# Kernel optimization log

Measured on AMD Instinct MI355X. Metric: run time of the kernel, lower is better.

The kernel has to match this reference:

```python
import jax, jax.numpy as jnp
import numpy as np

RCUT, RCUT_SMTH = 6.0, 0.5
SEL = [32, 64]
SEC = [0, 32, 96]
PAIRS = [(0, 0), (0, 1), (1, 1)]  # (ti, tj) with ti <= tj, matching stacked weight index
NF, NLOC, NALL = 1, 256, 512
NNEI = sum(SEL)
NG = 96


def setup_inputs() -> dict:
    key = jax.random.key(0)
    ks = jax.random.split(key, 10)
    # coords in a 4A cube so most neighbor distances are inside rcut=6
    extended_coord = jax.random.uniform(ks[0], (NF, NALL * 3), dtype=jnp.float32) * 4.0
    nl = jax.random.randint(ks[1], (NF, NLOC, NNEI), 0, NALL - 1)
    # shift indices >= own local index by 1 to avoid self-neighbors (zero distance)
    nlist = nl + (nl >= jnp.arange(NLOC)[None, :, None]).astype(nl.dtype)
    extended_atype = jax.random.randint(ks[2], (NF, NALL), 0, 2)
    mean = jnp.zeros((2, NNEI, 4), jnp.float32)
    stddev = jnp.ones((2, NNEI, 4), jnp.float32)
    def w(k, shape, fan):
        return jax.random.normal(k, shape, jnp.float32) / np.float32(np.sqrt(fan))
    W1 = w(ks[3], (3, 1, 24), 1.0)
    b1 = 0.1 * jax.random.normal(ks[4], (3, 24), jnp.float32)
    W2 = w(ks[5], (3, 24, 48), 24.0)
    b2 = 0.1 * jax.random.normal(ks[6], (3, 48), jnp.float32)
    W3 = w(ks[7], (3, 48, 96), 48.0)
    b3 = 0.1 * jax.random.normal(ks[8], (3, 96), jnp.float32)
    return dict(nlist=nlist, extended_coord=extended_coord, extended_atype=extended_atype,
                mean=mean, stddev=stddev, W1=W1, b1=b1, W2=W2, b2=b2, W3=W3, b3=b3)


def _smooth_weight(r, rmin, rmax):
    uu = (r - rmin) / (rmax - rmin)
    vv = uu * uu * uu * (-6.0 * uu * uu + 15.0 * uu - 10.0) + 1.0
    return jnp.where(r <= rmin, 1.0, jnp.where(r >= rmax, 0.0, vv))


def _env_mat(nlist, coord, atype, mean, stddev):
    nf, nloc, nnei = nlist.shape
    coord = coord.reshape(nf, -1, 3)
    mask = nlist >= 0
    nl = jnp.where(mask, nlist, 0)
    # gather neighbor coords: nf x nloc x nnei x 3
    coord_r = jnp.take_along_axis(coord, nl.reshape(nf, -1, 1), axis=1).reshape(nf, nloc, nnei, 3)
    diff = coord_r - coord[:, :nloc, None, :]
    length = jnp.linalg.norm(diff, axis=-1, keepdims=True)
    length = length + (~mask)[..., None].astype(diff.dtype)  # avoid 0-div on padded entries
    t0 = 1.0 / length
    t1 = diff / (length * length)
    sw = _smooth_weight(length, RCUT_SMTH, RCUT) * mask[..., None].astype(diff.dtype)
    env = jnp.concatenate([t0, t1], axis=-1) * sw  # nf x nloc x nnei x 4
    loc_type = atype[:, :nloc]
    dmatrix = (env - mean[loc_type]) / stddev[loc_type]
    return dmatrix, sw


def _embed(x, W1, b1, W2, b2, W3, b3):
    # EmbeddingNet 1->24->48->96, tanh, resnet doubling residuals
    h1 = jnp.tanh(x @ W1 + b1)
    h2 = jnp.tanh(h1 @ W2 + b2) + jnp.concatenate([h1, h1], axis=-1)
    h3 = jnp.tanh(h2 @ W3 + b3) + jnp.concatenate([h2, h2], axis=-1)
    return h3


def reference(nlist, extended_coord, extended_atype, mean, stddev, W1, b1, W2, b2, W3, b3):
    nf, nloc, nnei = nlist.shape
    dmatrix, sw = _env_mat(nlist, extended_coord, extended_atype, mean, stddev)
    dm = dmatrix.reshape(nf * nloc, nnei, 4)
    result = jnp.zeros((nf * nloc, NG), dm.dtype)
    for p, (ti, tj) in enumerate(PAIRS):
        rr_i = dm[:, SEC[ti]:SEC[ti + 1], 1:]  # nfnl x nt_i x 3
        rr_j = dm[:, SEC[tj]:SEC[tj + 1], 1:]  # nfnl x nt_j x 3
        env_ij = jnp.einsum('ijm,ikm->ijk', rr_i, rr_j)  # nfnl x nt_i x nt_j
        gg = _embed(env_ij[..., None], W1[p], b1[p], W2[p], b2[p], W3[p], b3[p])
        res_ij = jnp.einsum('ijk,ijkm->im', env_ij, gg)
        result = result + res_ij * (1.0 / (SEL[ti] * SEL[tj]))
    return result.reshape(nf, nloc, NG)
```

## Files before the change

### kernel.cpp

```cpp
#include <hip/hip_runtime.h>

#define NLOC 256
#define NNEI 96
#define NG   96
#define H1W  28
#define H2W  52
#define S2LE 2.88539008177793f

typedef __attribute__((ext_vector_type(8))) short short8;
typedef __attribute__((ext_vector_type(4))) float f32x4;
union Frag { uint4 u; short8 s; };

__device__ __forceinline__ float tanh_sc(float s) {
    float e = __builtin_amdgcn_exp2f(s);
    return 1.0f - 2.0f * __builtin_amdgcn_rcpf(e + 1.0f);
}
__device__ __forceinline__ unsigned short f2bf(float f) {
    unsigned int u = __float_as_uint(f);
    u += 0x7FFFu + ((u >> 16) & 1u);
    return (unsigned short)(u >> 16);
}
__device__ __forceinline__ unsigned short f2bf_rhu(float f) {
    return (unsigned short)((__float_as_uint(f) + 0x8000u) >> 16);
}
__device__ __forceinline__ unsigned int pack_bf2(float lo, float hi) {
    unsigned int a = __float_as_uint(lo) + 0x8000u;
    unsigned int b = __float_as_uint(hi) + 0x8000u;
    return __builtin_amdgcn_perm(b, a, 0x07060302);
}

__global__ __launch_bounds__(256) void prep_kernel(
        const float* __restrict__ W1, const float* __restrict__ b1,
        const float* __restrict__ W2, const float* __restrict__ b2,
        const float* __restrict__ W3, const float* __restrict__ b3,
        unsigned short* __restrict__ wf2, unsigned short* __restrict__ wf3,
        unsigned short* __restrict__ wfJ,
        float* __restrict__ w1s, float* __restrict__ b1s,
        float* __restrict__ b2s, float* __restrict__ b3s) {
    int t = blockIdx.x * blockDim.x + threadIdx.x;
    if (t < 2880) {
        int p = t / 960;
        int r = t % 960;
        int tile = r / 64;
        int l = r % 64;
        int nlo = l & 15, g = l >> 4;
        short8 v;
        if (tile < 3) {
            int nt = tile;
            #pragma unroll
            for (int j = 0; j < 8; j++) {
                int k = g * 8 + j;
                float w = (k < 24) ? W2[(p * 24 + k) * 48 + nt * 16 + nlo] * S2LE : 0.0f;
                v[j] = (short)f2bf(w);
            }
            *(short8*)(wf2 + ((p * 3 + nt) * 64 + l) * 8) = v;
        } else {
            int tt = tile - 3;
            int nt = tt >> 1, kc = tt & 1;
            #pragma unroll
            for (int j = 0; j < 8; j++) {
                int kk = (kc == 0) ? (g * 8 + j) : ((j < 4) ? (32 + g * 4 + j) : -1);
                float w = (kk >= 0) ? W3[(p * 48 + kk) * 96 + nt * 16 + nlo] * S2LE : 0.0f;
                v[j] = (short)f2bf(w);
            }
            *(short8*)(wf3 + ((p * 12 + nt * 2 + kc) * 64 + l) * 8) = v;
        }
    } else if (t < 3264) {
        int t2 = t - 2880;
        int f = t2 >> 6, l = t2 & 63;
        int ml = l & 15, g = l >> 4;
        short8 v;
        if (f < 3) {
            int c24 = (f * 16 + ml) % 24;
            #pragma unroll
            for (int j = 0; j < 8; j++)
                v[j] = (short)((g * 8 + j == c24) ? 0x3F80 : 0);
        } else {
            int nt2 = f - 3;
            if (nt2 < 2) {
                int c = nt2 * 16 + ml;
                #pragma unroll
                for (int j = 0; j < 8; j++)
                    v[j] = (short)((g * 8 + j == c) ? 0x3F80 : 0);
            } else {
                #pragma unroll
                for (int j = 0; j < 8; j++)
                    v[j] = (short)((j < 4 && (g * 4 + j) == ml) ? 0x3F80 : 0);
            }
        }
        *(short8*)(wfJ + (f * 64 + l) * 8) = v;
    } else if (t < 3768) {
        int u = t - 3264;
        if (u < 72)       { w1s[u] = W1[u] * S2LE; b1s[u] = b1[u] * S2LE; }
        else if (u < 216) { b2s[u - 72]  = b2[u - 72]  * S2LE; }
        else              { b3s[u - 216] = b3[u - 216] * S2LE; }
    }
}

__launch_bounds__(256, 4)
__global__ void mlp_kernel(const int* __restrict__ nlist, const float* __restrict__ coord,
                           const int* __restrict__ atype,
                           const float* __restrict__ mean, const float* __restrict__ stddev,
                           const float* __restrict__ w1s, const float* __restrict__ b1s,
                           const float* __restrict__ b2s, const float* __restrict__ b3s,
                           const unsigned short* __restrict__ wf2,
                           const unsigned short* __restrict__ wf3,
                           const unsigned short* __restrict__ wfJ,
                           float* __restrict__ out) {
    __shared__ __align__(16) unsigned char smem[40960];
    unsigned short* h1s = (unsigned short*)smem;
    unsigned short* h2s = (unsigned short*)(smem + 14336);
    float* rrl = (float*)(smem + 39808);
    unsigned char* h2b = (unsigned char*)h2s;

    int tid = threadIdx.x;
    int blk = blockIdx.x;
    int i = blk / 20;
    int b = blk - i * 20;

    int p, base_e, offi, offj, count, Aint;
    float scale;
    bool tri;
    if (b < 3)       { p=0; base_e=b*256;      offi=0;  offj=0;  scale=1.0f/1024.0f; count=528;  tri=true;  Aint=65;  }
    else if (b < 11) { p=1; base_e=(b-3)*256;  offi=0;  offj=32; scale=1.0f/2048.0f; count=2048; tri=false; Aint=0;   }
    else             { p=2; base_e=(b-11)*256; offi=32; offj=32; scale=1.0f/4096.0f; count=2080; tri=true;  Aint=129; }

    if (tid < NNEI) {
        int n = tid;
        int idx = nlist[i * NNEI + n];
        bool msk = idx >= 0;
        int safe = msk ? idx : 0;
        float cx = coord[i*3], cy = coord[i*3+1], cz = coord[i*3+2];
        float dx = coord[safe*3]   - cx;
        float dy = coord[safe*3+1] - cy;
        float dz = coord[safe*3+2] - cz;
        float rn = sqrtf(dx*dx + dy*dy + dz*dz) + (msk ? 0.0f : 1.0f);
        float sw;
        if (rn <= 0.5f)      sw = 1.0f;
        else if (rn >= 6.0f) sw = 0.0f;
        else {
            float uu = (rn - 0.5f) * (1.0f / 5.5f);
            sw = uu*uu*uu*(uu*(-6.0f*uu + 15.0f) - 10.0f) + 1.0f;
        }
        if (!msk) sw = 0.0f;
        float ir2 = 1.0f / (rn * rn);
        int ty = atype[i];
        const float* mu = mean   + (ty * NNEI + n) * 4;
        const float* sd = stddev + (ty * NNEI + n) * 4;
        rrl[n*3+0] = (dx * ir2 * sw - mu[1]) / sd[1];
        rrl[n*3+1] = (dy * ir2 * sw - mu[2]) / sd[2];
        rrl[n*3+2] = (dz * ir2 * sw - mu[3]) / sd[3];
    }
    __syncthreads();

    float xs;
    {
        int e = base_e + tid;
        bool valid = e < count;
        int ec = valid ? e : 0;
        int jj, kk;
        float mult = 1.0f;
        if (!tri) { jj = ec >> 6; kk = ec & 63; }
        else {
            float Af = (float)Aint;
            int j = (int)((Af - sqrtf(Af*Af - 8.0f*(float)ec)) * 0.5f);
            int Tj1 = ((j+1)*(Aint-j-1)) >> 1;
            if (ec >= Tj1) j++;
            int Tj = (j*(Aint-j)) >> 1;
            if (ec < Tj) { j--; Tj = (j*(Aint-j)) >> 1; }
            jj = j; kk = j + (ec - Tj);
            mult = (jj == kk) ? 1.0f : 2.0f;
        }
        const float* ri = rrl + (offi + jj) * 3;
        const float* rj = rrl + (offj + kk) * 3;
        float x = ri[0]*rj[0] + ri[1]*rj[1] + ri[2]*rj[2];
        x = valid ? x : 0.0f;
        xs = x * mult;

        const float* w1 = w1s + p * 24;
        const float* c1 = b1s + p * 24;
        float h1v[24];
        #pragma unroll
        for (int u = 0; u < 24; u++)
            h1v[u] = tanh_sc(fmaf(x, w1[u], c1[u]));
        #pragma unroll
        for (int t4 = 0; t4 < 6; t4++) {
            uint2 q = { pack_bf2(h1v[4*t4], h1v[4*t4+1]),
                        pack_bf2(h1v[4*t4+2], h1v[4*t4+3]) };
            *(uint2*)(h1s + tid*H1W + 4*t4) = q;
        }
        uint2 z2 = {0u, 0u};
        *(uint2*)(h1s + tid*H1W + 24) = z2;
        if (tid == 0) *(uint2*)h2s = z2;
    }
    __syncthreads();

    *(float*)(h2b + tid*104 + 96) = xs;
    if (tid < NG) *(float*)(h2b + tid*104 + 100) = 0.0f;

    int l  = tid & 63;
    int w  = tid >> 6;
    int ml = l & 15, g = l >> 4;

    short8 bw2[3], jf2[3];
    float  b2c[3];
    #pragma unroll
    for (int nt = 0; nt < 3; nt++) {
        bw2[nt] = *(const short8*)(wf2 + ((p*3 + nt)*64 + l)*8);
        jf2[nt] = *(const short8*)(wfJ + (nt*64 + l)*8);
        b2c[nt] = b2s[p*48 + nt*16 + ml];
    }
    #pragma unroll
    for (int mi = 0; mi < 4; mi++) {
        int mt = w*4 + mi;
        int arow = mt*16 + ml;
        uint2 lo = *(const uint2*)(h1s + arow*H1W + g*8);
        uint2 hi = *(const uint2*)(h1s + arow*H1W + g*8 + 4);
        Frag fa; fa.u = make_uint4(lo.x, lo.y, hi.x, hi.y);
        #pragma unroll
        for (int nt = 0; nt < 3; nt++) {
            f32x4 bini = {b2c[nt], b2c[nt], b2c[nt], b2c[nt]};
            f32x4 zz   = {0.f, 0.f, 0.f, 0.f};
            f32x4 acc = __builtin_amdgcn_mfma_f32_16x16x32_bf16(fa.s, bw2[nt], bini, 0, 0, 0);
            f32x4 aj  = __builtin_amdgcn_mfma_f32_16x16x32_bf16(fa.s, jf2[nt], zz,   0, 0, 0);
            int col = nt*16 + ml;
            #pragma unroll
            for (int r = 0; r < 4; r++) {
                int orow = mt*16 + g*4 + r;
                float v = tanh_sc(acc[r]) + aj[r];
                h2s[orow*H2W + col] = f2bf_rhu(v);
            }
        }
    }
    __syncthreads();

    short8 a3a[4], a3b[4];
    float  xv[4][4];
    #pragma unroll
    for (int mi = 0; mi < 4; mi++) {
        int mt = w*4 + mi;
        int arow = mt*16 + ml;
        uint2 lo = *(const uint2*)(h2s + arow*H2W + g*8);
        uint2 hi = *(const uint2*)(h2s + arow*H2W + g*8 + 4);
        Frag fa; fa.u = make_uint4(lo.x, lo.y, hi.x, hi.y);
        a3a[mi] = fa.s;
        uint2 t2 = *(const uint2*)(h2s + arow*H2W + 32 + g*4);
        Frag fb; fb.u = make_uint4(t2.x, t2.y, 0u, 0u);
        a3b[mi] = fb.s;
        #pragma unroll
        for (int r = 0; r < 4; r++)
            xv[mi][r] = *(const float*)(h2b + (mt*16 + g*4 + r)*104 + 96);
    }
    short8 jf3[3];
    #pragma unroll
    for (int q = 0; q < 3; q++)
        jf3[q] = *(const short8*)(wfJ + ((3 + q)*64 + l)*8);

    #pragma unroll
    for (int nt2 = 0; nt2 < 3; nt2++) {
        f32x4 zz = {0.f, 0.f, 0.f, 0.f};
        f32x4 aj[4];
        #pragma unroll
        for (int mi = 0; mi < 4; mi++)
            aj[mi] = __builtin_amdgcn_mfma_f32_16x16x32_bf16(
                (nt2 == 2) ? a3b[mi] : a3a[mi], jf3[nt2], zz, 0, 0, 0);
        #pragma unroll
        for (int h = 0; h < 2; h++) {
            int nt = nt2 + 3*h;
            short8 b30 = *(const short8*)(wf3 + ((p*12 + nt*2 + 0)*64 + l)*8);
            short8 b31 = *(const short8*)(wf3 + ((p*12 + nt*2 + 1)*64 + l)*8);
            float b3c = b3s[p*96 + nt*16 + ml];
            float facc = 0.0f;
            #pragma unroll
            for (int mi = 0; mi < 4; mi++) {
                f32x4 bini = {b3c, b3c, b3c, b3c};
                f32x4 acc = __builtin_amdgcn_mfma_f32_16x16x32_bf16(a3a[mi], b30, bini, 0, 0, 0);
                acc = __builtin_amdgcn_mfma_f32_16x16x32_bf16(a3b[mi], b31, acc, 0, 0, 0);
                #pragma unroll
                for (int r = 0; r < 4; r++) {
                    float h3 = tanh_sc(acc[r]) + aj[mi][r];
                    facc += xv[mi][r] * h3;
                }
            }
            facc += __shfl_xor(facc, 16, 64);
            facc += __shfl_xor(facc, 32, 64);
            if (g == 0) atomicAdd((float*)(h2b + (nt*16 + ml)*104 + 100), facc);
        }
    }
    __syncthreads();
    if (tid < NG)
        atomicAdd(&out[i*NG + tid], *(const float*)(h2b + tid*104 + 100) * scale);
}

extern "C" void kernel_launch(void* const* d_in, const int* in_sizes, int n_in,
                              void* d_out, int out_size, void* d_ws, size_t ws_size,
                              hipStream_t stream) {
    const int*   nlist  = (const int*)  d_in[0];
    const float* coord  = (const float*)d_in[1];
    const int*   atype  = (const int*)  d_in[2];
    const float* mean   = (const float*)d_in[3];
    const float* stddev = (const float*)d_in[4];
    const float* W1     = (const float*)d_in[5];
    const float* b1     = (const float*)d_in[6];
    const float* W2     = (const float*)d_in[7];
    const float* b2     = (const float*)d_in[8];
    const float* W3     = (const float*)d_in[9];
    const float* b3     = (const float*)d_in[10];
    float* out = (float*)d_out;

    char* ws = (char*)d_ws;
    unsigned short* wf2 = (unsigned short*)(ws + 0);
    unsigned short* wf3 = (unsigned short*)(ws + 9216);
    unsigned short* wfJ = (unsigned short*)(ws + 46080);
    float* w1s = (float*)(ws + 52224);
    float* b1s = (float*)(ws + 52512);
    float* b2s = (float*)(ws + 52800);
    float* b3s = (float*)(ws + 53376);

    prep_kernel<<<15, 256, 0, stream>>>(W1, b1, W2, b2, W3, b3,
                                        wf2, wf3, wfJ, w1s, b1s, b2s, b3s);
    mlp_kernel<<<NLOC * 20, 256, 0, stream>>>(
        nlist, coord, atype, mean, stddev,
        w1s, b1s, b2s, b3s, wf2, wf3, wfJ, out);
}
```

Before: 140.7 us.

## Replace block barriers with wave-local fences and compact LDS row layouts

Each wave now produces and consumes only its own rows of h1/h2, so the two block-wide __syncthreads are replaced by a per-wave lgkmcnt wait plus a scheduling barrier. The h1 row stride shrinks from 28 to 24 bf16 with 16-byte stores, and the zero padding is written up front with vector stores. The final tanh+residual is folded into exp/rcp/fma by pre-adding 1 to the residual term. The compact stride may add LDS bank conflicts, and correctness relies on every wave touching only its own rows, including the xs values written per thread.

```diff
diff --git a/kernel.cpp b/kernel.cpp
--- a/kernel.cpp
+++ b/kernel.cpp
@@ -3,8 +3,6 @@
 #define NLOC 256
 #define NNEI 96
 #define NG   96
-#define H1W  28
-#define H2W  52
 #define S2LE 2.88539008177793f
 
 typedef __attribute__((ext_vector_type(8))) short short8;
@@ -27,6 +25,10 @@
     unsigned int a = __float_as_uint(lo) + 0x8000u;
     unsigned int b = __float_as_uint(hi) + 0x8000u;
     return __builtin_amdgcn_perm(b, a, 0x07060302);
+}
+__device__ __forceinline__ void wave_fence() {
+    asm volatile("s_waitcnt lgkmcnt(0)" ::: "memory");
+    __builtin_amdgcn_sched_barrier(0);
 }
 
 __global__ __launch_bounds__(256) void prep_kernel(
@@ -107,10 +109,10 @@
                            const unsigned short* __restrict__ wf3,
                            const unsigned short* __restrict__ wfJ,
                            float* __restrict__ out) {
-    __shared__ __align__(16) unsigned char smem[40960];
+    __shared__ __align__(16) unsigned char smem[40080];
     unsigned short* h1s = (unsigned short*)smem;
-    unsigned short* h2s = (unsigned short*)(smem + 14336);
-    float* rrl = (float*)(smem + 39808);
+    unsigned short* h2s = (unsigned short*)(smem + 12304);
+    float* rrl = (float*)(smem + 38928);
     unsigned char* h2b = (unsigned char*)h2s;
 
     int tid = threadIdx.x;
@@ -125,6 +127,14 @@
     else if (b < 11) { p=1; base_e=(b-3)*256;  offi=0;  offj=32; scale=1.0f/2048.0f; count=2048; tri=false; Aint=0;   }
     else             { p=2; base_e=(b-11)*256; offi=32; offj=32; scale=1.0f/4096.0f; count=2080; tri=true;  Aint=129; }
 
+    {
+        uint4 z = make_uint4(0u, 0u, 0u, 0u);
+        *(uint4*)(smem + tid * 48 +  0) = z;
+        *(uint4*)(smem + tid * 48 + 16) = z;
+        *(uint4*)(smem + tid * 48 + 32) = z;
+        if (tid == 0) *(uint4*)(smem + 12288) = z;
+        if (tid < NG) *(float*)(h2b + tid * 104 + 100) = 0.0f;
+    }
     if (tid < NNEI) {
         int n = tid;
         int idx = nlist[i * NNEI + n];
@@ -184,19 +194,16 @@
         for (int u = 0; u < 24; u++)
             h1v[u] = tanh_sc(fmaf(x, w1[u], c1[u]));
         #pragma unroll
-        for (int t4 = 0; t4 < 6; t4++) {
-            uint2 q = { pack_bf2(h1v[4*t4], h1v[4*t4+1]),
-                        pack_bf2(h1v[4*t4+2], h1v[4*t4+3]) };
-            *(uint2*)(h1s + tid*H1W + 4*t4) = q;
-        }
-        uint2 z2 = {0u, 0u};
-        *(uint2*)(h1s + tid*H1W + 24) = z2;
-        if (tid == 0) *(uint2*)h2s = z2;
-    }
-    __syncthreads();
-
+        for (int t8 = 0; t8 < 3; t8++) {
+            uint4 q = make_uint4(pack_bf2(h1v[8*t8+0], h1v[8*t8+1]),
+                                 pack_bf2(h1v[8*t8+2], h1v[8*t8+3]),
+                                 pack_bf2(h1v[8*t8+4], h1v[8*t8+5]),
+                                 pack_bf2(h1v[8*t8+6], h1v[8*t8+7]));
+            *(uint4*)(h1s + tid*24 + 8*t8) = q;
+        }
+    }
     *(float*)(h2b + tid*104 + 96) = xs;
-    if (tid < NG) *(float*)(h2b + tid*104 + 100) = 0.0f;
+    wave_fence();
 
     int l  = tid & 63;
     int w  = tid >> 6;
@@ -214,8 +221,8 @@
     for (int mi = 0; mi < 4; mi++) {
         int mt = w*4 + mi;
         int arow = mt*16 + ml;
-        uint2 lo = *(const uint2*)(h1s + arow*H1W + g*8);
-        uint2 hi = *(const uint2*)(h1s + arow*H1W + g*8 + 4);
+        uint2 lo = *(const uint2*)(h1s + arow*24 + g*8);
+        uint2 hi = *(const uint2*)(h1s + arow*24 + g*8 + 4);
         Frag fa; fa.u = make_uint4(lo.x, lo.y, hi.x, hi.y);
         #pragma unroll
         for (int nt = 0; nt < 3; nt++) {
@@ -228,11 +235,11 @@
             for (int r = 0; r < 4; r++) {
                 int orow = mt*16 + g*4 + r;
                 float v = tanh_sc(acc[r]) + aj[r];
-                h2s[orow*H2W + col] = f2bf_rhu(v);
-            }
-        }
-    }
-    __syncthreads();
+                h2s[orow*52 + col] = f2bf_rhu(v);
+            }
+        }
+    }
+    wave_fence();
 
     short8 a3a[4], a3b[4];
     float  xv[4][4];
@@ -240,11 +247,11 @@
     for (int mi = 0; mi < 4; mi++) {
         int mt = w*4 + mi;
         int arow = mt*16 + ml;
-        uint2 lo = *(const uint2*)(h2s + arow*H2W + g*8);
-        uint2 hi = *(const uint2*)(h2s + arow*H2W + g*8 + 4);
+        uint2 lo = *(const uint2*)(h2s + arow*52 + g*8);
+        uint2 hi = *(const uint2*)(h2s + arow*52 + g*8 + 4);
         Frag fa; fa.u = make_uint4(lo.x, lo.y, hi.x, hi.y);
         a3a[mi] = fa.s;
-        uint2 t2 = *(const uint2*)(h2s + arow*H2W + 32 + g*4);
+        uint2 t2 = *(const uint2*)(h2s + arow*52 + 32 + g*4);
         Frag fb; fb.u = make_uint4(t2.x, t2.y, 0u, 0u);
         a3b[mi] = fb.s;
         #pragma unroll
@@ -259,11 +266,13 @@
     #pragma unroll
     for (int nt2 = 0; nt2 < 3; nt2++) {
         f32x4 zz = {0.f, 0.f, 0.f, 0.f};
-        f32x4 aj[4];
-        #pragma unroll
-        for (int mi = 0; mi < 4; mi++)
-            aj[mi] = __builtin_amdgcn_mfma_f32_16x16x32_bf16(
+        f32x4 ajp[4];
+        #pragma unroll
+        for (int mi = 0; mi < 4; mi++) {
+            f32x4 a = __builtin_amdgcn_mfma_f32_16x16x32_bf16(
                 (nt2 == 2) ? a3b[mi] : a3a[mi], jf3[nt2], zz, 0, 0, 0);
+            ajp[mi] = a + 1.0f;
+        }
         #pragma unroll
         for (int h = 0; h < 2; h++) {
             int nt = nt2 + 3*h;
@@ -278,8 +287,10 @@
                 acc = __builtin_amdgcn_mfma_f32_16x16x32_bf16(a3b[mi], b31, acc, 0, 0, 0);
                 #pragma unroll
                 for (int r = 0; r < 4; r++) {
-                    float h3 = tanh_sc(acc[r]) + aj[mi][r];
-                    facc += xv[mi][r] * h3;
+                    float e2 = __builtin_amdgcn_exp2f(acc[r]);
+                    float rc = __builtin_amdgcn_rcpf(e2 + 1.0f);
+                    float h3 = fmaf(-2.0f, rc, ajp[mi][r]);
+                    facc = fmaf(xv[mi][r], h3, facc);
                 }
             }
             facc += __shfl_xor(facc, 16, 64);
```

Measured after the change: 138.7 us. Within noise of the previous version (-1.4%).
